# Optimization experiments

Hardware: AMD Instinct MI355X
Metric: run time of the kernel (lower is better)

The kernel has to match this reference:

```python
import jax, jax.numpy as jnp
import numpy as np

WS = 7          # window_size (square)
HEADS = 12


def _relative_position_index(ws=WS):
    # Faithful port of WindowAttentionBase._get_relative_position_index
    coords = np.stack(np.meshgrid(np.arange(ws), np.arange(ws), indexing='ij'))  # [2, ws, ws]
    flat = coords.reshape(2, -1)                       # [2, n]
    rel = flat[:, :, None] - flat[:, None, :]          # [2, n, n]
    rel = rel.transpose(1, 2, 0)                       # [n, n, 2]
    rel[:, :, 0] += ws - 1
    rel[:, :, 1] += ws - 1
    rel[:, :, 0] *= 2 * ws - 1
    return jnp.asarray(rel.sum(-1).reshape(-1), dtype=jnp.int32)  # [n*n]


def setup_inputs() -> dict:
    key = jax.random.key(0)
    ks = jax.random.split(key, 6)
    b, H, W, c = 32, 56, 56, 384
    return {
        "x": jax.random.normal(ks[0], (b, H, W, c), jnp.float32),
        "w_qkv": jax.random.normal(ks[1], (3 * c, c), jnp.float32) * (c ** -0.5),
        "b_qkv": jax.random.normal(ks[2], (3 * c,), jnp.float32) * 0.02,
        "rel_pos": jax.random.normal(ks[3], (HEADS, (2 * WS - 1) ** 2), jnp.float32),
        "w_out": jax.random.normal(ks[4], (c, c), jnp.float32) * (c ** -0.5),
        "b_out": jax.random.normal(ks[5], (c,), jnp.float32) * 0.02,
    }


def reference(x, w_qkv, b_qkv, rel_pos, w_out, b_out):
    b, H, W, c = x.shape
    g = HEADS
    d = c // g
    hn, wn = H // WS, W // WS
    n = WS * WS
    scale = d ** -0.5

    # split_into_windows: 'b (p h) (q w) c -> b h w (p q) c'  (p,q = window dims, OUTER factors)
    xw = x.reshape(b, WS, hn, WS, wn, c).transpose(0, 2, 4, 1, 3, 5).reshape(b, hn, wn, n, c)

    qkv = xw @ w_qkv.T + b_qkv                          # [b, hn, wn, n, 3c]
    q, k, v = jnp.split(qkv, 3, axis=-1)
    # 'b h w n (g d) -> b g h w n d'
    to_heads = lambda t: t.reshape(b, hn, wn, n, g, d).transpose(0, 4, 1, 2, 3, 5)
    q, k, v = to_heads(q) * scale, to_heads(k), to_heads(v)

    sim = jnp.einsum('bghwnd,bghwmd->bghwnm', q, k)     # [b, g, hn, wn, n, n]
    idx = _relative_position_index()
    bias = rel_pos[:, idx].reshape(g, n, n)             # gather relative position bias
    sim = sim + bias[None, :, None, None, :, :]

    attn = jax.nn.softmax(sim, axis=-1)
    out = jnp.einsum('bghwnm,bghwmd->bghwnd', attn, v)  # [b, g, hn, wn, n, d]

    # 'b g h w n d -> b h w n (g d)' then merge_windows 'b h w (p q) c -> b (p h) (q w) c'
    out = out.transpose(0, 2, 3, 4, 1, 5).reshape(b, hn, wn, n, c)
    out = out.reshape(b, hn, wn, WS, WS, c).transpose(0, 3, 1, 4, 2, 5).reshape(b, H, W, c)
    return out @ w_out.T + b_out
```

## Files before the change

kernel.cpp:

```cpp
#include <hip/hip_runtime.h>

typedef __attribute__((ext_vector_type(8))) short bf16x8;
typedef __attribute__((ext_vector_type(4))) float f32x4;

__device__ __forceinline__ unsigned short f2bf(float f){
  unsigned u = __builtin_bit_cast(unsigned, f);
  u += 0x7fffu + ((u >> 16) & 1u);
  return (unsigned short)(u >> 16);
}

__device__ __forceinline__ unsigned cvt_pk_bf16(float lo, float hi){
  unsigned r;
  asm("v_cvt_pk_bf16_f32 %0, %1, %2" : "=v"(r) : "v"(lo), "v"(hi));
  return r;
}

#define ASYNC16(ldsp, gp) __builtin_amdgcn_global_load_lds( \
    (const __attribute__((address_space(1))) unsigned int*)(gp), \
    (__attribute__((address_space(3))) unsigned int*)(ldsp), 16, 0, 0)

__global__ __launch_bounds__(256) void prep_kernel(const float* __restrict__ x,
                                                   const float* __restrict__ wq,
                                                   const float* __restrict__ wo,
                                                   const float* __restrict__ rel_pos,
                                                   unsigned short* __restrict__ xb,
                                                   unsigned short* __restrict__ wqb,
                                                   unsigned short* __restrict__ wob,
                                                   float* __restrict__ btab){
  const int bid = blockIdx.x;
  if (bid < 37632){
    int idx = bid*256 + threadIdx.x;
    int token = idx / 96, j = idx - token*96;
    int b = token / 3136, rem = token - b*3136;
    int rr = rem / 56, cp = rem - rr*56;
    int p = rr >> 3, h = rr & 7, q = cp >> 3, w = cp & 7;
    int orow = ((b*8 + h)*8 + w)*49 + p*7 + q;
    float4 v = *(const float4*)(x + (size_t)idx*4);
    ushort4 o;
    o.x = f2bf(v.x); o.y = f2bf(v.y); o.z = f2bf(v.z); o.w = f2bf(v.w);
    *(ushort4*)(xb + (size_t)orow*384 + j*4) = o;
  } else if (bid < 38208){
    int idx = (bid - 37632)*256 + threadIdx.x;
    if (idx < 110592){
      float4 v = *(const float4*)(wq + (size_t)idx*4);
      ushort4 o; o.x=f2bf(v.x); o.y=f2bf(v.y); o.z=f2bf(v.z); o.w=f2bf(v.w);
      *(ushort4*)(wqb + (size_t)idx*4) = o;
    } else {
      int k = idx - 110592;
      float4 v = *(const float4*)(wo + (size_t)k*4);
      ushort4 o; o.x=f2bf(v.x); o.y=f2bf(v.y); o.z=f2bf(v.z); o.w=f2bf(v.w);
      *(ushort4*)(wob + (size_t)k*4) = o;
    }
  } else {
    int idx = (bid - 38208)*256 + threadIdx.x;
    int head = idx >> 10, rem = idx & 1023;
    int fi = rem >> 6, lane = rem & 63;
    int ti = fi >> 2, tj = fi & 3;
    int qq = tj*16 + (lane & 15);
    int kb = ti*16 + (lane >> 4)*4;
    float4 v; float* vp = (float*)&v;
#pragma unroll
    for (int r=0; r<4; ++r){
      int kk = kb + r;
      float val;
      if (kk >= 49) val = -__builtin_inff();
      else if (qq >= 49) val = 0.f;
      else {
        int ip = qq/7, iq = qq - ip*7, jp = kk/7, jq = kk - jp*7;
        val = rel_pos[head*169 + (ip-jp+6)*13 + (iq-jq+6)] * 1.4426950408889634f;
      }
      vp[r] = val;
    }
    *(float4*)(btab + (size_t)idx*4) = v;
  }
}

template<int EPI, int NBY>
__global__ __launch_bounds__(256) void gemm256(const unsigned short* __restrict__ A,
                                               const unsigned short* __restrict__ B,
                                               const float* __restrict__ bias,
                                               unsigned short* __restrict__ qo,
                                               unsigned short* __restrict__ ko,
                                               unsigned short* __restrict__ vo,
                                               float* __restrict__ out)
{
  constexpr int K = 384;
  constexpr int NT = 12;
  __shared__ unsigned short Al[3][256*32];
  __shared__ unsigned short Bl[3][128*32];
  const int tid = threadIdx.x;
  const int lane = tid & 63, wid = tid >> 6;
  const int wr = wid >> 1, wc = wid & 1;
  const int l15 = lane & 15, kg = lane >> 4;
  const int swz = (l15 >> 1) & 3;
  const int cswz = (tid & 3) ^ ((tid >> 3) & 3);

  const int n = blockIdx.x;
  const int xcd = n & 7, s = n >> 3;
  const int panel = s / NBY, nb = s - panel*NBY;
  const int bx = panel*8 + xcd, by = nb;

  const unsigned short* Ag = A + ((size_t)bx*256 + (tid>>2))*K + cswz*8;
  const unsigned short* Bg = B + ((size_t)(by*128 + (tid>>2)))*K + cswz*8;

  f32x4 acc[8][4] = {};

#define STAGE(buf, kt) do { \
    ASYNC16(&Al[buf][wid*512],        Ag + (kt)*32); \
    ASYNC16(&Al[buf][wid*512 + 2048], Ag + (size_t)64*K  + (kt)*32); \
    ASYNC16(&Al[buf][wid*512 + 4096], Ag + (size_t)128*K + (kt)*32); \
    ASYNC16(&Al[buf][wid*512 + 6144], Ag + (size_t)192*K + (kt)*32); \
    ASYNC16(&Bl[buf][wid*512],        Bg + (kt)*32); \
    ASYNC16(&Bl[buf][wid*512 + 2048], Bg + (size_t)64*K  + (kt)*32); \
  } while(0)

  STAGE(0,0); STAGE(1,1);

#pragma unroll
  for (int t = 0; t < NT; ++t){
    if (t < NT-1) asm volatile("s_waitcnt vmcnt(6)\n\ts_barrier" ::: "memory");
    else          asm volatile("s_waitcnt vmcnt(0)\n\ts_barrier" ::: "memory");

    if (t + 2 < NT) STAGE((t+2)%3, t+2);

    const unsigned short* Ab = Al[t % 3];
    const unsigned short* Bb = Bl[t % 3];
    bf16x8 af[8], bfv[4];
#pragma unroll
    for (int ti=0; ti<8; ++ti)
      af[ti] = *(const bf16x8*)(Ab + (wr*128 + ti*16 + l15)*32 + (kg ^ swz)*8);
#pragma unroll
    for (int tj=0; tj<4; ++tj)
      bfv[tj] = *(const bf16x8*)(Bb + (wc*64 + tj*16 + l15)*32 + (kg ^ swz)*8);

    __builtin_amdgcn_s_setprio(1);
#pragma unroll
    for (int ti=0; ti<8; ++ti)
#pragma unroll
      for (int tj=0; tj<4; ++tj)
        acc[ti][tj] = __builtin_amdgcn_mfma_f32_16x16x32_bf16(af[ti], bfv[tj], acc[ti][tj], 0,0,0);
    __builtin_amdgcn_s_setprio(0);
  }
#undef STAGE

  const int rbase = bx*256 + wr*128 + kg*4;

  if (EPI == 0){
    const int t = by / 3;
    unsigned short* __restrict__ Pout = (t==0) ? qo : ((t==1) ? ko : vo);
    const float scale = (t==0) ? (0.17677669529663689f * 1.4426950408889634f) : 1.0f;
    const int cb = (by - t*3)*128 + wc*64;
    int hoff[4]; float bvs[4];
#pragma unroll
    for (int tj=0; tj<4; ++tj){
      int colt = cb + tj*16;
      hoff[tj] = (colt>>5)*1568 + (colt&31) + l15;
      bvs[tj] = bias[by*128 + wc*64 + tj*16 + l15] * scale;
    }
#pragma unroll
    for (int ti=0; ti<8; ++ti){
#pragma unroll
      for (int r=0; r<4; ++r){
        int R = rbase + ti*16 + r;
        int win = R / 49, nn = R - win*49;
        size_t rowoff = (size_t)win*18816 + nn*32;
#pragma unroll
        for (int tj=0; tj<4; ++tj)
          Pout[rowoff + hoff[tj]] = f2bf(acc[ti][tj][r]*scale + bvs[tj]);
      }
    }
  } else {
    const int cbs = by*128 + wc*64;
    float bv[4];
#pragma unroll
    for (int tj=0; tj<4; ++tj) bv[tj] = bias[cbs + tj*16 + l15];
#pragma unroll
    for (int ti=0; ti<8; ++ti){
#pragma unroll
      for (int r=0; r<4; ++r){
        int R = rbase + ti*16 + r;
        int win = R / 49, nn = R - win*49;
        int p = nn / 7, q = nn - p*7;
        int h = (win >> 3) & 7, w = win & 7;
        size_t tok = (size_t)(win >> 6)*3136 + (size_t)((p*8 + h)*56 + q*8 + w);
        float* __restrict__ orow = out + tok*384 + cbs + l15;
#pragma unroll
        for (int tj=0; tj<4; ++tj)
          orow[tj*16] = acc[ti][tj][r] + bv[tj];
      }
    }
  }
}

__global__ __launch_bounds__(256) void attn_kernel(const unsigned short* __restrict__ q,
                                                   const unsigned short* __restrict__ k,
                                                   const unsigned short* __restrict__ v,
                                                   const float* __restrict__ btab,
                                                   unsigned short* __restrict__ ao)
{
  __shared__ unsigned short P[4][4096];
  const int tid = threadIdx.x, lane = tid & 63, wid = tid >> 6;
  const int l15 = lane & 15, kg = lane >> 4;
  const int win = blockIdx.x / 3;
  const int head = (blockIdx.x % 3)*4 + wid;
  const size_t base = ((size_t)win*12 + head)*1568;
  const unsigned short* qb = q + base;
  const unsigned short* kb = k + base;
  const unsigned short* vb = v + base;
  const float* bt = btab + head*4096;

  bf16x8 vfk[2][2];
#pragma unroll
  for (int ks=0; ks<2; ++ks)
#pragma unroll
    for (int tjv=0; tjv<2; ++tjv)
#pragma unroll
      for (int e=0; e<8; ++e)
        vfk[ks][tjv][e] = (short)vb[(ks*32 + kg*8 + e)*32 + tjv*16 + l15];

  f32x4 s[4][4];
#pragma unroll
  for (int ti=0; ti<4; ++ti)
#pragma unroll
    for (int tj=0; tj<4; ++tj)
      s[ti][tj] = *(const f32x4*)(bt + ((ti*4 + tj)*64 + lane)*4);

  bf16x8 kf[4], qf[4];
#pragma unroll
  for (int ti=0; ti<4; ++ti) kf[ti] = *(const bf16x8*)(kb + (ti*16+l15)*32 + kg*8);
#pragma unroll
  for (int tj=0; tj<4; ++tj) qf[tj] = *(const bf16x8*)(qb + (tj*16+l15)*32 + kg*8);

  __builtin_amdgcn_s_setprio(1);
#pragma unroll
  for (int ti=0; ti<4; ++ti)
#pragma unroll
    for (int tj=0; tj<4; ++tj)
      s[ti][tj] = __builtin_amdgcn_mfma_f32_16x16x32_bf16(kf[ti], qf[tj], s[ti][tj], 0,0,0);
  __builtin_amdgcn_s_setprio(0);

  float rinv[4];
#pragma unroll
  for (int tj=0; tj<4; ++tj){
    float sum = 0.f;
#pragma unroll
    for (int ti=0; ti<4; ++ti)
#pragma unroll
      for (int r=0; r<4; ++r){
        float e = exp2f(s[ti][tj][r]);
        s[ti][tj][r] = e;
        sum += e;
      }
    sum += __shfl_xor(sum, 16);
    sum += __shfl_xor(sum, 32);
    rinv[tj] = __builtin_amdgcn_rcpf(sum);
  }

  unsigned short* Pl = P[wid];
  const unsigned swz = (unsigned)((l15 & 7) << 4);
#pragma unroll
  for (int tj=0; tj<4; ++tj){
    const float rv = rinv[tj];
    const unsigned rowb = (unsigned)((tj*16 + l15)*128);
#pragma unroll
    for (int ti=0; ti<4; ++ti){
      uint2 d;
      d.x = cvt_pk_bf16(s[ti][tj][0]*rv, s[ti][tj][1]*rv);
      d.y = cvt_pk_bf16(s[ti][tj][2]*rv, s[ti][tj][3]*rv);
      unsigned boff = (rowb + (unsigned)(ti*32 + kg*8)) ^ swz;
      *(uint2*)((char*)Pl + boff) = d;
    }
  }

  f32x4 o[4][2] = {};
#pragma unroll
  for (int oti=0; oti<4; ++oti){
    bf16x8 pa[2];
#pragma unroll
    for (int ks=0; ks<2; ++ks){
      unsigned boff = ((unsigned)((oti*16+l15)*128 + ks*64 + kg*16)) ^ swz;
      pa[ks] = *(const bf16x8*)((char*)Pl + boff);
    }
    __builtin_amdgcn_s_setprio(1);
#pragma unroll
    for (int tjv=0; tjv<2; ++tjv){
      o[oti][tjv] = __builtin_amdgcn_mfma_f32_16x16x32_bf16(pa[0], vfk[0][tjv], o[oti][tjv], 0,0,0);
      o[oti][tjv] = __builtin_amdgcn_mfma_f32_16x16x32_bf16(pa[1], vfk[1][tjv], o[oti][tjv], 0,0,0);
    }
    __builtin_amdgcn_s_setprio(0);
  }

#pragma unroll
  for (int oti=0; oti<4; ++oti)
#pragma unroll
    for (int r=0; r<4; ++r){
      int row = oti*16 + kg*4 + r;
      if (row < 49){
        unsigned short* op = ao + ((size_t)win*49 + row)*384 + head*32 + l15;
        op[0]  = (unsigned short)cvt_pk_bf16(o[oti][0][r], o[oti][0][r]);
        op[16] = (unsigned short)cvt_pk_bf16(o[oti][1][r], o[oti][1][r]);
      }
    }
}

extern "C" void kernel_launch(void* const* d_in, const int* in_sizes, int n_in,
                              void* d_out, int out_size, void* d_ws, size_t ws_size,
                              hipStream_t stream)
{
  const float* x       = (const float*)d_in[0];
  const float* w_qkv   = (const float*)d_in[1];
  const float* b_qkv   = (const float*)d_in[2];
  const float* rel_pos = (const float*)d_in[3];
  const float* w_out   = (const float*)d_in[4];
  const float* b_out   = (const float*)d_in[5];
  float* out = (float*)d_out;

  char* ws = (char*)d_ws;
  unsigned short* wqb = (unsigned short*)ws;
  unsigned short* wob = (unsigned short*)(ws + 884736);
  float* btab         = (float*)(ws + 884736 + 294912);
  unsigned short* qws = (unsigned short*)(ws + 1376256);
  unsigned short* kws = qws + 38535168;
  unsigned short* vws = kws + 38535168;
  unsigned short* xb  = vws + 38535168;
  unsigned short* ao  = xb;

  prep_kernel<<<dim3(38256), dim3(256), 0, stream>>>(x, w_qkv, w_out, rel_pos,
                                                     xb, wqb, wob, btab);
  gemm256<0,9><<<dim3(3528), dim3(256), 0, stream>>>(xb, wqb, b_qkv, qws, kws, vws, nullptr);
  attn_kernel<<<dim3(6144), dim3(256), 0, stream>>>(qws, kws, vws, btab, ao);
  gemm256<1,3><<<dim3(1176), dim3(256), 0, stream>>>(ao, wob, b_out, nullptr, nullptr, nullptr, out);
}
```

Before: 303.2 us.

## Pre-swizzle weights into MFMA fragment layout and load B directly to registers

The prep kernel now writes the bf16 weight matrices in a fragment-major layout matching the MFMA B-operand register layout. The GEMM then loads B fragments straight from global memory into double-buffered registers instead of staging them through LDS, which removes the B LDS buffers and their LDS reads. This cuts LDS traffic and footprint, which may allow higher occupancy, at the cost of more outstanding global loads per wave and a waitcnt accounting that relies on the ordering of the register loads.

```diff
diff --git a/kernel.cpp b/kernel.cpp
--- a/kernel.cpp
+++ b/kernel.cpp
@@ -39,20 +39,29 @@
     ushort4 o;
     o.x = f2bf(v.x); o.y = f2bf(v.y); o.z = f2bf(v.z); o.w = f2bf(v.w);
     *(ushort4*)(xb + (size_t)orow*384 + j*4) = o;
-  } else if (bid < 38208){
+  } else if (bid < 37920){
     int idx = (bid - 37632)*256 + threadIdx.x;
-    if (idx < 110592){
-      float4 v = *(const float4*)(wq + (size_t)idx*4);
-      ushort4 o; o.x=f2bf(v.x); o.y=f2bf(v.y); o.z=f2bf(v.z); o.w=f2bf(v.w);
-      *(ushort4*)(wqb + (size_t)idx*4) = o;
-    } else {
-      int k = idx - 110592;
-      float4 v = *(const float4*)(wo + (size_t)k*4);
-      ushort4 o; o.x=f2bf(v.x); o.y=f2bf(v.y); o.z=f2bf(v.z); o.w=f2bf(v.w);
-      *(ushort4*)(wob + (size_t)k*4) = o;
-    }
+    const float* src;
+    unsigned short* dst;
+    int slot;
+    if (idx < 55296){ slot = idx;         src = wq; dst = wqb + (size_t)idx*8; }
+    else            { slot = idx - 55296; src = wo; dst = wob + (size_t)(idx-55296)*8; }
+    int lane = slot & 63;
+    int r = slot >> 6;
+    int tj = r & 3; r >>= 2;
+    int t = r % 12, bw = r / 12;
+    int row = bw*64 + tj*16 + (lane & 15);
+    int col = t*32 + (lane >> 4)*8;
+    const float* s = src + (size_t)row*384 + col;
+    float4 v1 = *(const float4*)(s);
+    float4 v2 = *(const float4*)(s + 4);
+    ushort4 o1, o2;
+    o1.x=f2bf(v1.x); o1.y=f2bf(v1.y); o1.z=f2bf(v1.z); o1.w=f2bf(v1.w);
+    o2.x=f2bf(v2.x); o2.y=f2bf(v2.y); o2.z=f2bf(v2.z); o2.w=f2bf(v2.w);
+    *(ushort4*)(dst)     = o1;
+    *(ushort4*)(dst + 4) = o2;
   } else {
-    int idx = (bid - 38208)*256 + threadIdx.x;
+    int idx = (bid - 37920)*256 + threadIdx.x;
     int head = idx >> 10, rem = idx & 1023;
     int fi = rem >> 6, lane = rem & 63;
     int ti = fi >> 2, tj = fi & 3;
@@ -87,7 +96,6 @@
   constexpr int K = 384;
   constexpr int NT = 12;
   __shared__ unsigned short Al[3][256*32];
-  __shared__ unsigned short Bl[3][128*32];
   const int tid = threadIdx.x;
   const int lane = tid & 63, wid = tid >> 6;
   const int wr = wid >> 1, wc = wid & 1;
@@ -101,47 +109,52 @@
   const int bx = panel*8 + xcd, by = nb;
 
   const unsigned short* Ag = A + ((size_t)bx*256 + (tid>>2))*K + cswz*8;
-  const unsigned short* Bg = B + ((size_t)(by*128 + (tid>>2)))*K + cswz*8;
+  const unsigned short* Bf = B + ((size_t)(by*2 + wc))*12*2048 + lane*8;
 
   f32x4 acc[8][4] = {};
+  bf16x8 bfr[2][4];
 
 #define STAGE(buf, kt) do { \
     ASYNC16(&Al[buf][wid*512],        Ag + (kt)*32); \
     ASYNC16(&Al[buf][wid*512 + 2048], Ag + (size_t)64*K  + (kt)*32); \
     ASYNC16(&Al[buf][wid*512 + 4096], Ag + (size_t)128*K + (kt)*32); \
     ASYNC16(&Al[buf][wid*512 + 6144], Ag + (size_t)192*K + (kt)*32); \
-    ASYNC16(&Bl[buf][wid*512],        Bg + (kt)*32); \
-    ASYNC16(&Bl[buf][wid*512 + 2048], Bg + (size_t)64*K  + (kt)*32); \
   } while(0)
-
-  STAGE(0,0); STAGE(1,1);
+#define LOADB(d, kt) do { \
+    bfr[d][0] = *(const bf16x8*)(Bf + (kt)*2048); \
+    bfr[d][1] = *(const bf16x8*)(Bf + (kt)*2048 + 512); \
+    bfr[d][2] = *(const bf16x8*)(Bf + (kt)*2048 + 1024); \
+    bfr[d][3] = *(const bf16x8*)(Bf + (kt)*2048 + 1536); \
+  } while(0)
+
+  STAGE(0,0); LOADB(0,0);
+  STAGE(1,1); LOADB(1,1);
 
 #pragma unroll
   for (int t = 0; t < NT; ++t){
-    if (t < NT-1) asm volatile("s_waitcnt vmcnt(6)\n\ts_barrier" ::: "memory");
+    if (t < NT-1) asm volatile("s_waitcnt vmcnt(8)\n\ts_barrier" ::: "memory");
     else          asm volatile("s_waitcnt vmcnt(0)\n\ts_barrier" ::: "memory");
 
     if (t + 2 < NT) STAGE((t+2)%3, t+2);
 
     const unsigned short* Ab = Al[t % 3];
-    const unsigned short* Bb = Bl[t % 3];
-    bf16x8 af[8], bfv[4];
+    bf16x8 af[8];
 #pragma unroll
     for (int ti=0; ti<8; ++ti)
       af[ti] = *(const bf16x8*)(Ab + (wr*128 + ti*16 + l15)*32 + (kg ^ swz)*8);
-#pragma unroll
-    for (int tj=0; tj<4; ++tj)
-      bfv[tj] = *(const bf16x8*)(Bb + (wc*64 + tj*16 + l15)*32 + (kg ^ swz)*8);
 
     __builtin_amdgcn_s_setprio(1);
 #pragma unroll
     for (int ti=0; ti<8; ++ti)
 #pragma unroll
       for (int tj=0; tj<4; ++tj)
-        acc[ti][tj] = __builtin_amdgcn_mfma_f32_16x16x32_bf16(af[ti], bfv[tj], acc[ti][tj], 0,0,0);
+        acc[ti][tj] = __builtin_amdgcn_mfma_f32_16x16x32_bf16(af[ti], bfr[t&1][tj], acc[ti][tj], 0,0,0);
     __builtin_amdgcn_s_setprio(0);
+
+    if (t + 2 < NT) LOADB(t&1, t+2);
   }
 #undef STAGE
+#undef LOADB
 
   const int rbase = bx*256 + wr*128 + kg*4;
 
@@ -325,7 +338,7 @@
   unsigned short* xb  = vws + 38535168;
   unsigned short* ao  = xb;
 
-  prep_kernel<<<dim3(38256), dim3(256), 0, stream>>>(x, w_qkv, w_out, rel_pos,
+  prep_kernel<<<dim3(37968), dim3(256), 0, stream>>>(x, w_qkv, w_out, rel_pos,
                                                      xb, wqb, wob, btab);
   gemm256<0,9><<<dim3(3528), dim3(256), 0, stream>>>(xb, wqb, b_qkv, qws, kws, vws, nullptr);
   attn_kernel<<<dim3(6144), dim3(256), 0, stream>>>(qws, kws, vws, btab, ao);
```

After: 344.7 us. 13.7% more time.

## Fuse QKV projection into windowed attention kernel, dropping Q/K/V global round trip

Applied to the files above, without the earlier changes.

The QKV GEMM and the attention kernel are merged into one kernel. Each block computes Q, K and V for one window and four heads straight from the bf16 input using MFMA, stages them through LDS, and runs softmax attention without writing Q/K/V to global memory. The prep kernel now pre-swizzles w_qkv into MFMA fragment order so B fragments can be read directly from global memory. This removes roughly 230MB of Q/K/V write and read traffic and one launch. In exchange the GEMM loses its LDS tiling and reuse: A fragments are read from global or cache three times per window (once per head group), and the 49-row windows are padded to 64, which wastes MFMA work.

```diff
diff --git a/kernel.cpp b/kernel.cpp
--- a/kernel.cpp
+++ b/kernel.cpp
@@ -39,20 +39,33 @@
     ushort4 o;
     o.x = f2bf(v.x); o.y = f2bf(v.y); o.z = f2bf(v.z); o.w = f2bf(v.w);
     *(ushort4*)(xb + (size_t)orow*384 + j*4) = o;
-  } else if (bid < 38208){
+  } else if (bid < 37992){
     int idx = (bid - 37632)*256 + threadIdx.x;
-    if (idx < 110592){
-      float4 v = *(const float4*)(wq + (size_t)idx*4);
-      ushort4 o; o.x=f2bf(v.x); o.y=f2bf(v.y); o.z=f2bf(v.z); o.w=f2bf(v.w);
-      *(ushort4*)(wqb + (size_t)idx*4) = o;
+    if (idx < 55296){
+      int lane = idx & 63;
+      int r = idx >> 6;
+      int wt = r & 7; int r2 = r >> 3;
+      int t = r2 % 12, gi = r2 / 12;
+      int hgp = gi / 3, m = gi - hgp*3;
+      int row = m*384 + hgp*128 + (wt>>1)*32 + (wt&1)*16 + (lane & 15);
+      int col = t*32 + (lane >> 4)*8;
+      const float* s = wq + (size_t)row*384 + col;
+      float4 v1 = *(const float4*)(s);
+      float4 v2 = *(const float4*)(s + 4);
+      ushort4 o1, o2;
+      o1.x=f2bf(v1.x); o1.y=f2bf(v1.y); o1.z=f2bf(v1.z); o1.w=f2bf(v1.w);
+      o2.x=f2bf(v2.x); o2.y=f2bf(v2.y); o2.z=f2bf(v2.z); o2.w=f2bf(v2.w);
+      unsigned short* dst = wqb + (size_t)idx*8;
+      *(ushort4*)(dst)     = o1;
+      *(ushort4*)(dst + 4) = o2;
     } else {
-      int k = idx - 110592;
+      int k = idx - 55296;
       float4 v = *(const float4*)(wo + (size_t)k*4);
       ushort4 o; o.x=f2bf(v.x); o.y=f2bf(v.y); o.z=f2bf(v.z); o.w=f2bf(v.w);
       *(ushort4*)(wob + (size_t)k*4) = o;
     }
   } else {
-    int idx = (bid - 38208)*256 + threadIdx.x;
+    int idx = (bid - 37992)*256 + threadIdx.x;
     int head = idx >> 10, rem = idx & 1023;
     int fi = rem >> 6, lane = rem & 63;
     int ti = fi >> 2, tj = fi & 3;
@@ -75,13 +88,210 @@
   }
 }
 
-template<int EPI, int NBY>
+__global__ __launch_bounds__(256, 2) void fqa_kernel(const unsigned short* __restrict__ xb,
+                                                     const unsigned short* __restrict__ Wf,
+                                                     const float* __restrict__ bqkv,
+                                                     const float* __restrict__ btab,
+                                                     unsigned short* __restrict__ ao)
+{
+  __shared__ unsigned short QK[4][4096];
+  __shared__ unsigned short VT[4][2048];
+  __shared__ unsigned short P [4][4096];
+  const int tid = threadIdx.x, lane = tid & 63, wid = tid >> 6;
+  const int l15 = lane & 15, kg = lane >> 4;
+  const int win = blockIdx.x & 2047;
+  const int hg  = blockIdx.x >> 11;
+  const int head = hg*4 + wid;
+
+  const unsigned short* ap[4];
+#pragma unroll
+  for (int ti=0; ti<4; ++ti){
+    int rowg = win*49 + ti*16 + l15;
+    if (rowg > 100351) rowg = 100351;
+    ap[ti] = xb + (size_t)rowg*384 + kg*8;
+  }
+  const unsigned short* bp[3][2];
+#pragma unroll
+  for (int m=0; m<3; ++m)
+#pragma unroll
+    for (int tjj=0; tjj<2; ++tjj)
+      bp[m][tjj] = Wf + ((size_t)((hg*3 + m)*12)*8 + wid*2 + tjj)*512 + lane*8;
+
+  f32x4 aq[4][2] = {}, ak[4][2] = {}, av[4][2] = {};
+  bf16x8 afr[2][4], bq[2][2], bk[2][2], bv[2][2];
+
+#define LOADA(d, t) do { \
+    afr[d][0] = *(const bf16x8*)(ap[0] + (t)*32); \
+    afr[d][1] = *(const bf16x8*)(ap[1] + (t)*32); \
+    afr[d][2] = *(const bf16x8*)(ap[2] + (t)*32); \
+    afr[d][3] = *(const bf16x8*)(ap[3] + (t)*32); \
+  } while(0)
+#define LOADB(d, t) do { \
+    bq[d][0] = *(const bf16x8*)(bp[0][0] + (t)*4096); \
+    bq[d][1] = *(const bf16x8*)(bp[0][1] + (t)*4096); \
+    bk[d][0] = *(const bf16x8*)(bp[1][0] + (t)*4096); \
+    bk[d][1] = *(const bf16x8*)(bp[1][1] + (t)*4096); \
+    bv[d][0] = *(const bf16x8*)(bp[2][0] + (t)*4096); \
+    bv[d][1] = *(const bf16x8*)(bp[2][1] + (t)*4096); \
+  } while(0)
+
+  LOADA(0, 0); LOADB(0, 0);
+#pragma unroll
+  for (int t=0; t<12; ++t){
+    const int cur = t & 1;
+    if (t < 11){ LOADA(cur^1, t+1); LOADB(cur^1, t+1); }
+    __builtin_amdgcn_s_setprio(1);
+#pragma unroll
+    for (int ti=0; ti<4; ++ti)
+#pragma unroll
+      for (int tjj=0; tjj<2; ++tjj){
+        aq[ti][tjj] = __builtin_amdgcn_mfma_f32_16x16x32_bf16(afr[cur][ti], bq[cur][tjj], aq[ti][tjj], 0,0,0);
+        ak[ti][tjj] = __builtin_amdgcn_mfma_f32_16x16x32_bf16(afr[cur][ti], bk[cur][tjj], ak[ti][tjj], 0,0,0);
+        av[ti][tjj] = __builtin_amdgcn_mfma_f32_16x16x32_bf16(afr[cur][ti], bv[cur][tjj], av[ti][tjj], 0,0,0);
+      }
+    __builtin_amdgcn_s_setprio(0);
+  }
+#undef LOADA
+#undef LOADB
+
+  const float SCL = 0.17677669529663689f * 1.4426950408889634f;
+  float biasq[2], biask[2], biasv[2];
+#pragma unroll
+  for (int tjj=0; tjj<2; ++tjj){
+    int col = hg*128 + wid*32 + tjj*16 + l15;
+    biasq[tjj] = bqkv[col] * SCL;
+    biask[tjj] = bqkv[384 + col];
+    biasv[tjj] = bqkv[768 + col];
+  }
+
+  unsigned short* QKl = QK[wid];
+  unsigned short* VTl = VT[wid];
+#pragma unroll
+  for (int ti=0; ti<4; ++ti){
+#pragma unroll
+    for (int tjj=0; tjj<2; ++tjj){
+      const int cq = tjj*2 + (l15 >> 3);
+      const int ck = 4 + tjj*2 + (l15 >> 3);
+      const int sub = (l15 & 7)*2;
+#pragma unroll
+      for (int r=0; r<4; ++r){
+        int tok = ti*16 + kg*4 + r;
+        unsigned oq = (unsigned)(tok*128 + ((cq ^ (tok & 7)) << 4) + sub);
+        unsigned ok = (unsigned)(tok*128 + ((ck ^ (tok & 7)) << 4) + sub);
+        *(unsigned short*)((char*)QKl + oq) = f2bf(aq[ti][tjj][r]*SCL + biasq[tjj]);
+        *(unsigned short*)((char*)QKl + ok) = f2bf(ak[ti][tjj][r] + biask[tjj]);
+      }
+      int dd = tjj*16 + l15;
+      int cb = ti*2 + (kg >> 1);
+      uint2 d;
+      d.x = cvt_pk_bf16(av[ti][tjj][0] + biasv[tjj], av[ti][tjj][1] + biasv[tjj]);
+      d.y = cvt_pk_bf16(av[ti][tjj][2] + biasv[tjj], av[ti][tjj][3] + biasv[tjj]);
+      unsigned ov = (unsigned)(dd*128 + ((cb ^ (dd & 7)) << 4) + (kg & 1)*8);
+      *(uint2*)((char*)VTl + ov) = d;
+    }
+  }
+
+  const float* bt = btab + head*4096;
+  f32x4 s[4][4];
+#pragma unroll
+  for (int ti=0; ti<4; ++ti)
+#pragma unroll
+    for (int tj=0; tj<4; ++tj)
+      s[ti][tj] = *(const f32x4*)(bt + ((ti*4 + tj)*64 + lane)*4);
+
+  bf16x8 kf[4], qf[4];
+#pragma unroll
+  for (int i=0; i<4; ++i){
+    int tok = i*16 + l15;
+    qf[i] = *(const bf16x8*)((char*)QKl + tok*128 + ((kg       ^ (tok & 7)) << 4));
+    kf[i] = *(const bf16x8*)((char*)QKl + tok*128 + (((4 + kg) ^ (tok & 7)) << 4));
+  }
+
+  __builtin_amdgcn_s_setprio(1);
+#pragma unroll
+  for (int ti=0; ti<4; ++ti)
+#pragma unroll
+    for (int tj=0; tj<4; ++tj)
+      s[ti][tj] = __builtin_amdgcn_mfma_f32_16x16x32_bf16(kf[ti], qf[tj], s[ti][tj], 0,0,0);
+  __builtin_amdgcn_s_setprio(0);
+
+  float rinv[4];
+#pragma unroll
+  for (int tj=0; tj<4; ++tj){
+    float sum = 0.f;
+#pragma unroll
+    for (int ti=0; ti<4; ++ti)
+#pragma unroll
+      for (int r=0; r<4; ++r){
+        float e = exp2f(s[ti][tj][r]);
+        s[ti][tj][r] = e;
+        sum += e;
+      }
+    sum += __shfl_xor(sum, 16);
+    sum += __shfl_xor(sum, 32);
+    rinv[tj] = __builtin_amdgcn_rcpf(sum);
+  }
+
+  unsigned short* Pl = P[wid];
+  const unsigned swzP = (unsigned)((l15 & 7) << 4);
+#pragma unroll
+  for (int tj=0; tj<4; ++tj){
+    const float rv = rinv[tj];
+    const unsigned rowb = (unsigned)((tj*16 + l15)*128);
+#pragma unroll
+    for (int ti=0; ti<4; ++ti){
+      uint2 d;
+      d.x = cvt_pk_bf16(s[ti][tj][0]*rv, s[ti][tj][1]*rv);
+      d.y = cvt_pk_bf16(s[ti][tj][2]*rv, s[ti][tj][3]*rv);
+      unsigned boff = (rowb + (unsigned)(ti*32 + kg*8)) ^ swzP;
+      *(uint2*)((char*)Pl + boff) = d;
+    }
+  }
+
+  bf16x8 vfk[2][2];
+#pragma unroll
+  for (int ks=0; ks<2; ++ks)
+#pragma unroll
+    for (int tjv=0; tjv<2; ++tjv){
+      int dd = tjv*16 + l15;
+      vfk[ks][tjv] = *(const bf16x8*)((char*)VTl + dd*128 + (((ks*4 + kg) ^ (dd & 7)) << 4));
+    }
+
+  f32x4 o[4][2] = {};
+#pragma unroll
+  for (int oti=0; oti<4; ++oti){
+    bf16x8 pa[2];
+#pragma unroll
+    for (int ks=0; ks<2; ++ks){
+      unsigned boff = ((unsigned)((oti*16 + l15)*128 + ks*64 + kg*16)) ^ swzP;
+      pa[ks] = *(const bf16x8*)((char*)Pl + boff);
+    }
+    __builtin_amdgcn_s_setprio(1);
+#pragma unroll
+    for (int tjv=0; tjv<2; ++tjv){
+      o[oti][tjv] = __builtin_amdgcn_mfma_f32_16x16x32_bf16(pa[0], vfk[0][tjv], o[oti][tjv], 0,0,0);
+      o[oti][tjv] = __builtin_amdgcn_mfma_f32_16x16x32_bf16(pa[1], vfk[1][tjv], o[oti][tjv], 0,0,0);
+    }
+    __builtin_amdgcn_s_setprio(0);
+  }
+
+#pragma unroll
+  for (int oti=0; oti<4; ++oti)
+#pragma unroll
+    for (int r=0; r<4; ++r){
+      int row = oti*16 + kg*4 + r;
+      if (row < 49){
+        unsigned short* op = ao + ((size_t)win*49 + row)*384 + head*32 + l15;
+        op[0]  = (unsigned short)cvt_pk_bf16(o[oti][0][r], o[oti][0][r]);
+        op[16] = (unsigned short)cvt_pk_bf16(o[oti][1][r], o[oti][1][r]);
+      }
+    }
+}
+
+template<int NBY>
 __global__ __launch_bounds__(256) void gemm256(const unsigned short* __restrict__ A,
                                                const unsigned short* __restrict__ B,
                                                const float* __restrict__ bias,
-                                               unsigned short* __restrict__ qo,
-                                               unsigned short* __restrict__ ko,
-                                               unsigned short* __restrict__ vo,
                                                float* __restrict__ out)
 {
   constexpr int K = 384;
@@ -144,163 +354,25 @@
 #undef STAGE
 
   const int rbase = bx*256 + wr*128 + kg*4;
-
-  if (EPI == 0){
-    const int t = by / 3;
-    unsigned short* __restrict__ Pout = (t==0) ? qo : ((t==1) ? ko : vo);
-    const float scale = (t==0) ? (0.17677669529663689f * 1.4426950408889634f) : 1.0f;
-    const int cb = (by - t*3)*128 + wc*64;
-    int hoff[4]; float bvs[4];
-#pragma unroll
-    for (int tj=0; tj<4; ++tj){
-      int colt = cb + tj*16;
-      hoff[tj] = (colt>>5)*1568 + (colt&31) + l15;
-      bvs[tj] = bias[by*128 + wc*64 + tj*16 + l15] * scale;
-    }
-#pragma unroll
-    for (int ti=0; ti<8; ++ti){
-#pragma unroll
-      for (int r=0; r<4; ++r){
-        int R = rbase + ti*16 + r;
-        int win = R / 49, nn = R - win*49;
-        size_t rowoff = (size_t)win*18816 + nn*32;
-#pragma unroll
-        for (int tj=0; tj<4; ++tj)
-          Pout[rowoff + hoff[tj]] = f2bf(acc[ti][tj][r]*scale + bvs[tj]);
-      }
-    }
-  } else {
-    const int cbs = by*128 + wc*64;
-    float bv[4];
-#pragma unroll
-    for (int tj=0; tj<4; ++tj) bv[tj] = bias[cbs + tj*16 + l15];
-#pragma unroll
-    for (int ti=0; ti<8; ++ti){
-#pragma unroll
-      for (int r=0; r<4; ++r){
-        int R = rbase + ti*16 + r;
-        int win = R / 49, nn = R - win*49;
-        int p = nn / 7, q = nn - p*7;
-        int h = (win >> 3) & 7, w = win & 7;
-        size_t tok = (size_t)(win >> 6)*3136 + (size_t)((p*8 + h)*56 + q*8 + w);
-        float* __restrict__ orow = out + tok*384 + cbs + l15;
-#pragma unroll
-        for (int tj=0; tj<4; ++tj)
-          orow[tj*16] = acc[ti][tj][r] + bv[tj];
-      }
-    }
-  }
-}
-
-__global__ __launch_bounds__(256) void attn_kernel(const unsigned short* __restrict__ q,
-                                                   const unsigned short* __restrict__ k,
-                                                   const unsigned short* __restrict__ v,
-                                                   const float* __restrict__ btab,
-                                                   unsigned short* __restrict__ ao)
-{
-  __shared__ unsigned short P[4][4096];
-  const int tid = threadIdx.x, lane = tid & 63, wid = tid >> 6;
-  const int l15 = lane & 15, kg = lane >> 4;
-  const int win = blockIdx.x / 3;
-  const int head = (blockIdx.x % 3)*4 + wid;
-  const size_t base = ((size_t)win*12 + head)*1568;
-  const unsigned short* qb = q + base;
-  const unsigned short* kb = k + base;
-  const unsigned short* vb = v + base;
-  const float* bt = btab + head*4096;
-
-  bf16x8 vfk[2][2];
-#pragma unroll
-  for (int ks=0; ks<2; ++ks)
-#pragma unroll
-    for (int tjv=0; tjv<2; ++tjv)
-#pragma unroll
-      for (int e=0; e<8; ++e)
-        vfk[ks][tjv][e] = (short)vb[(ks*32 + kg*8 + e)*32 + tjv*16 + l15];
-
-  f32x4 s[4][4];
-#pragma unroll
-  for (int ti=0; ti<4; ++ti)
-#pragma unroll
-    for (int tj=0; tj<4; ++tj)
-      s[ti][tj] = *(const f32x4*)(bt + ((ti*4 + tj)*64 + lane)*4);
-
-  bf16x8 kf[4], qf[4];
-#pragma unroll
-  for (int ti=0; ti<4; ++ti) kf[ti] = *(const bf16x8*)(kb + (ti*16+l15)*32 + kg*8);
-#pragma unroll
-  for (int tj=0; tj<4; ++tj) qf[tj] = *(const bf16x8*)(qb + (tj*16+l15)*32 + kg*8);
-
-  __builtin_amdgcn_s_setprio(1);
-#pragma unroll
-  for (int ti=0; ti<4; ++ti)
-#pragma unroll
-    for (int tj=0; tj<4; ++tj)
-      s[ti][tj] = __builtin_amdgcn_mfma_f32_16x16x32_bf16(kf[ti], qf[tj], s[ti][tj], 0,0,0);
-  __builtin_amdgcn_s_setprio(0);
-
-  float rinv[4];
-#pragma unroll
-  for (int tj=0; tj<4; ++tj){
-    float sum = 0.f;
-#pragma unroll
-    for (int ti=0; ti<4; ++ti)
-#pragma unroll
-      for (int r=0; r<4; ++r){
-        float e = exp2f(s[ti][tj][r]);
-        s[ti][tj][r] = e;
-        sum += e;
-      }
-    sum += __shfl_xor(sum, 16);
-    sum += __shfl_xor(sum, 32);
-    rinv[tj] = __builtin_amdgcn_rcpf(sum);
-  }
-
-  unsigned short* Pl = P[wid];
-  const unsigned swz = (unsigned)((l15 & 7) << 4);
-#pragma unroll
-  for (int tj=0; tj<4; ++tj){
-    const float rv = rinv[tj];
-    const unsigned rowb = (unsigned)((tj*16 + l15)*128);
-#pragma unroll
-    for (int ti=0; ti<4; ++ti){
-      uint2 d;
-      d.x = cvt_pk_bf16(s[ti][tj][0]*rv, s[ti][tj][1]*rv);
-      d.y = cvt_pk_bf16(s[ti][tj][2]*rv, s[ti][tj][3]*rv);
-      unsigned boff = (rowb + (unsigned)(ti*32 + kg*8)) ^ swz;
-      *(uint2*)((char*)Pl + boff) = d;
-    }
-  }
-
-  f32x4 o[4][2] = {};
-#pragma unroll
-  for (int oti=0; oti<4; ++oti){
-    bf16x8 pa[2];
-#pragma unroll
-    for (int ks=0; ks<2; ++ks){
-      unsigned boff = ((unsigned)((oti*16+l15)*128 + ks*64 + kg*16)) ^ swz;
-      pa[ks] = *(const bf16x8*)((char*)Pl + boff);
-    }
-    __builtin_amdgcn_s_setprio(1);
-#pragma unroll
-    for (int tjv=0; tjv<2; ++tjv){
-      o[oti][tjv] = __builtin_amdgcn_mfma_f32_16x16x32_bf16(pa[0], vfk[0][tjv], o[oti][tjv], 0,0,0);
-      o[oti][tjv] = __builtin_amdgcn_mfma_f32_16x16x32_bf16(pa[1], vfk[1][tjv], o[oti][tjv], 0,0,0);
-    }
-    __builtin_amdgcn_s_setprio(0);
-  }
-
-#pragma unroll
-  for (int oti=0; oti<4; ++oti)
+  const int cbs = by*128 + wc*64;
+  float bv[4];
+#pragma unroll
+  for (int tj=0; tj<4; ++tj) bv[tj] = bias[cbs + tj*16 + l15];
+#pragma unroll
+  for (int ti=0; ti<8; ++ti){
 #pragma unroll
     for (int r=0; r<4; ++r){
-      int row = oti*16 + kg*4 + r;
-      if (row < 49){
-        unsigned short* op = ao + ((size_t)win*49 + row)*384 + head*32 + l15;
-        op[0]  = (unsigned short)cvt_pk_bf16(o[oti][0][r], o[oti][0][r]);
-        op[16] = (unsigned short)cvt_pk_bf16(o[oti][1][r], o[oti][1][r]);
-      }
-    }
+      int R = rbase + ti*16 + r;
+      int win = R / 49, nn = R - win*49;
+      int p = nn / 7, q = nn - p*7;
+      int h = (win >> 3) & 7, w = win & 7;
+      size_t tok = (size_t)(win >> 6)*3136 + (size_t)((p*8 + h)*56 + q*8 + w);
+      float* __restrict__ orow = out + tok*384 + cbs + l15;
+#pragma unroll
+      for (int tj=0; tj<4; ++tj)
+        orow[tj*16] = acc[ti][tj][r] + bv[tj];
+    }
+  }
 }
 
 extern "C" void kernel_launch(void* const* d_in, const int* in_sizes, int n_in,
@@ -319,15 +391,11 @@
   unsigned short* wqb = (unsigned short*)ws;
   unsigned short* wob = (unsigned short*)(ws + 884736);
   float* btab         = (float*)(ws + 884736 + 294912);
-  unsigned short* qws = (unsigned short*)(ws + 1376256);
-  unsigned short* kws = qws + 38535168;
-  unsigned short* vws = kws + 38535168;
-  unsigned short* xb  = vws + 38535168;
-  unsigned short* ao  = xb;
-
-  prep_kernel<<<dim3(38256), dim3(256), 0, stream>>>(x, w_qkv, w_out, rel_pos,
+  unsigned short* xb  = (unsigned short*)(ws + 1376256);
+  unsigned short* ao  = xb + 38535168;
+
+  prep_kernel<<<dim3(38040), dim3(256), 0, stream>>>(x, w_qkv, w_out, rel_pos,
                                                      xb, wqb, wob, btab);
-  gemm256<0,9><<<dim3(3528), dim3(256), 0, stream>>>(xb, wqb, b_qkv, qws, kws, vws, nullptr);
-  attn_kernel<<<dim3(6144), dim3(256), 0, stream>>>(qws, kws, vws, btab, ao);
-  gemm256<1,3><<<dim3(1176), dim3(256), 0, stream>>>(ao, wob, b_out, nullptr, nullptr, nullptr, out);
-}
+  fqa_kernel<<<dim3(6144), dim3(256), 0, stream>>>(xb, wqb, b_qkv, btab, ao);
+  gemm256<3><<<dim3(1176), dim3(256), 0, stream>>>(ao, wob, b_out, out);
+}
```

New measurement: 306.6 us. Within noise of the previous version (+1.1%).
